# Performance work log

Measured on AMD Instinct MI355X. Metric: run time of the kernel, lower is better.

Reference implementation:

```python
import jax, jax.numpy as jnp
import numpy as np

IN_F = 1024
OUT_F = 1024
DEGREE = 7  # degree+1 = 8 Chebyshev terms


def setup_inputs() -> dict:
    key = jax.random.key(0)
    k1, k2, k3 = jax.random.split(key, 3)
    x = jax.random.normal(k1, (16384, IN_F), dtype=jnp.float32)
    std = 1.0 / (IN_F * (DEGREE + 1))
    cheby_coeffs = jax.random.normal(k2, (OUT_F, IN_F, DEGREE + 1), dtype=jnp.float32) * std
    # xavier_uniform for base_weight [out, in]
    limit = float(np.sqrt(6.0 / (IN_F + OUT_F)))
    base_weight = jax.random.uniform(k3, (OUT_F, IN_F), dtype=jnp.float32, minval=-limit, maxval=limit)
    return {"x": x, "cheby_coeffs": cheby_coeffs, "base_weight": base_weight}


def _cheby_basis(x_norm, degree):
    terms = [jnp.ones_like(x_norm), x_norm]
    for _ in range(2, degree + 1):
        terms.append(2.0 * x_norm * terms[-1] - terms[-2])
    return jnp.stack(terms, axis=-1)  # [b, i, d+1]


def reference(x, cheby_coeffs, base_weight):
    x_norm = jnp.tanh(x)
    basis = _cheby_basis(x_norm, DEGREE)               # [b, i, d]
    kan_out = jnp.einsum('bid,oid->bo', basis, cheby_coeffs)
    base_out = x @ base_weight.T                        # F.linear
    return kan_out + base_out
```

## Files before the change

kernel.cpp:

```cpp
#include <hip/hip_runtime.h>
#include <hip/hip_bf16.h>
#include <stdint.h>

typedef short short8 __attribute__((ext_vector_type(8)));
typedef float f32x16 __attribute__((ext_vector_type(16)));

#define KD 8192
#define NT 128

__device__ __forceinline__ unsigned short bfb(float f) {
    __hip_bfloat16 h = __float2bfloat16(f);
    return __builtin_bit_cast(unsigned short, h);
}

__device__ __forceinline__ short8 cheby8(float xv) {
    float e  = __builtin_amdgcn_exp2f(xv * 2.8853900817779268f);
    float xn = 1.0f - 2.0f * __builtin_amdgcn_rcpf(1.0f + e);
    float x2 = xn + xn;
    float t2 = x2 * xn - 1.0f;
    float t3 = x2 * t2 - xn;
    float t4 = x2 * t3 - t2;
    float t5 = x2 * t4 - t3;
    float t6 = x2 * t5 - t4;
    float t7 = x2 * t6 - t5;
    short8 v;
    v[0] = bfb(xv); v[1] = bfb(xn); v[2] = bfb(t2); v[3] = bfb(t3);
    v[4] = bfb(t4); v[5] = bfb(t5); v[6] = bfb(t6); v[7] = bfb(t7);
    return v;
}

__global__ void prep_w(const float* __restrict__ C, const float* __restrict__ W,
                       unsigned short* __restrict__ Bw) {
    int g = blockIdx.x * 256 + threadIdx.x;
    int o = g >> 10, i = g & 1023;
    const float* src = C + ((size_t)o * 8192 + i * 8);
    float4 v0 = *(const float4*)src;
    float4 v1 = *(const float4*)(src + 4);
    v0.x = W[o * 1024 + i];
    short8 r;
    r[0] = bfb(v0.x); r[1] = bfb(v0.y); r[2] = bfb(v0.z); r[3] = bfb(v0.w);
    r[4] = bfb(v1.x); r[5] = bfb(v1.y); r[6] = bfb(v1.z); r[7] = bfb(v1.w);
    *(short8*)(Bw + (size_t)g * 8) = r;
}

__global__ void prep_bias(const float* __restrict__ C, float* __restrict__ bias) {
    int o = blockIdx.x;
    int tid = threadIdx.x;
    float s = 0.f;
    for (int i = tid; i < 1024; i += 256)
        s += C[(size_t)o * 8192 + (size_t)i * 8];
    #pragma unroll
    for (int off = 32; off > 0; off >>= 1) s += __shfl_down(s, off);
    __shared__ float red[4];
    if ((tid & 63) == 0) red[tid >> 6] = s;
    __syncthreads();
    if (tid == 0) bias[o] = red[0] + red[1] + red[2] + red[3];
}


#define GLDS(NXT_, C_, TT_) \
    __builtin_amdgcn_global_load_lds( \
        (const __attribute__((address_space(1))) unsigned int*)((const char*)Bw + boff[C_] + (size_t)(TT_) * 128), \
        (__attribute__((address_space(3))) unsigned int*)(&Bs[NXT_][(wave * 4 + (C_)) * 8][0]), 16, 0, 0)

#define XLOAD(DST_, TI_) { \
    const float* ap_ = xbase + (size_t)(TI_) * 8; \
    asm volatile("global_load_dwordx4 %0, %1, off" : "=&v"(DST_) : "v"(ap_)); }

#define PHASE(CUR_, KK_) { \
    const int fb_ = (KK_) * 2 + lg; \
    const int co_ = (fb_ ^ (lr & 7)) * 16; \
    short8 a0_ = *(const short8*)((const char*)&As[CUR_][0][0] + (wm +  0 + lr) * 128 + co_); \
    short8 a1_ = *(const short8*)((const char*)&As[CUR_][0][0] + (wm + 32 + lr) * 128 + co_); \
    short8 a2_ = *(const short8*)((const char*)&As[CUR_][0][0] + (wm + 64 + lr) * 128 + co_); \
    short8 a3_ = *(const short8*)((const char*)&As[CUR_][0][0] + (wm + 96 + lr) * 128 + co_); \
    short8 b0_ = *(const short8*)((const char*)&Bs[CUR_][0][0] + (wn +  0 + lr) * 128 + co_); \
    short8 b1_ = *(const short8*)((const char*)&Bs[CUR_][0][0] + (wn + 32 + lr) * 128 + co_); \
    __builtin_amdgcn_s_setprio(1); \
    acc[0][0] = __builtin_amdgcn_mfma_f32_32x32x16_bf16(a0_, b0_, acc[0][0], 0, 0, 0); \
    acc[0][1] = __builtin_amdgcn_mfma_f32_32x32x16_bf16(a0_, b1_, acc[0][1], 0, 0, 0); \
    acc[1][0] = __builtin_amdgcn_mfma_f32_32x32x16_bf16(a1_, b0_, acc[1][0], 0, 0, 0); \
    acc[1][1] = __builtin_amdgcn_mfma_f32_32x32x16_bf16(a1_, b1_, acc[1][1], 0, 0, 0); \
    acc[2][0] = __builtin_amdgcn_mfma_f32_32x32x16_bf16(a2_, b0_, acc[2][0], 0, 0, 0); \
    acc[2][1] = __builtin_amdgcn_mfma_f32_32x32x16_bf16(a2_, b1_, acc[2][1], 0, 0, 0); \
    acc[3][0] = __builtin_amdgcn_mfma_f32_32x32x16_bf16(a3_, b0_, acc[3][0], 0, 0, 0); \
    acc[3][1] = __builtin_amdgcn_mfma_f32_32x32x16_bf16(a3_, b1_, acc[3][1], 0, 0, 0); \
    __builtin_amdgcn_s_setprio(0); \
}

#define CHEBY_STAGE(NXT_, XV_) { \
    short8 c0_ = cheby8(XV_.x); \
    short8 c1_ = cheby8(XV_.y); \
    short8 c2_ = cheby8(XV_.z); \
    short8 c3_ = cheby8(XV_.w); \
    *(short8*)((char*)&As[NXT_][0][0] + woff[0]) = c0_; \
    *(short8*)((char*)&As[NXT_][0][0] + woff[1]) = c1_; \
    *(short8*)((char*)&As[NXT_][0][0] + woff[2]) = c2_; \
    *(short8*)((char*)&As[NXT_][0][0] + woff[3]) = c3_; \
}

#define TILE(CUR_, NXT_, T_, XU_, XL_) { \
    const int tn_ = ((T_) + 1 < NT) ? (T_) + 1 : NT - 1; \
    const int tl_ = ((T_) + 2 < NT) ? (T_) + 2 : NT - 1; \
    GLDS(NXT_, 0, tn_); GLDS(NXT_, 1, tn_); GLDS(NXT_, 2, tn_); GLDS(NXT_, 3, tn_); \
    XLOAD(XL_, tl_) \
    PHASE(CUR_, 0) \
    PHASE(CUR_, 1) \
    asm volatile("s_waitcnt vmcnt(5)" ::: "memory");  \
    __builtin_amdgcn_sched_barrier(0); \
    CHEBY_STAGE(NXT_, XU_) \
    PHASE(CUR_, 2) \
    PHASE(CUR_, 3) \
    asm volatile("s_waitcnt vmcnt(1)" ::: "memory");  \
    __builtin_amdgcn_sched_barrier(0); \
    asm volatile("s_waitcnt lgkmcnt(0)" ::: "memory");  \
    __builtin_amdgcn_s_barrier(); \
    __builtin_amdgcn_sched_barrier(0); \
}

__global__ __launch_bounds__(512, 2)
void cheby_gemm(const float* __restrict__ X, const unsigned short* __restrict__ Bw,
                const float* __restrict__ bias, float* __restrict__ Out) {
    __shared__ unsigned short As[2][256][64];
    __shared__ unsigned short Bs[2][256][64];

    const int tid  = threadIdx.x;
    const int lane = tid & 63;
    const int wave = tid >> 6;

    int bid = blockIdx.x;
    int lin = (bid & 7) * 32 + (bid >> 3);
    const int m0 = (lin & 63) << 8;
    const int n0 = (lin >> 6) << 8;

    const int wm = (wave >> 2) * 128;
    const int wn = (wave & 3) * 64;
    const int lr = lane & 31;
    const int lg = lane >> 5;

    const int arow = tid >> 1;
    const int xf   = (tid & 1) * 4;
    const float* xbase = X + (size_t)(m0 + arow) * 1024 + xf;
    unsigned int woff[4];
    #pragma unroll
    for (int j = 0; j < 4; ++j)
        woff[j] = (unsigned)(arow * 128 + (((xf + j) ^ (arow & 7)) * 16));

    unsigned int boff[4];
    #pragma unroll
    for (int c = 0; c < 4; ++c) {
        int row   = (wave * 4 + c) * 8 + (lane >> 3);
        int chunk = (lane & 7) ^ (lane >> 3);
        boff[c] = ((unsigned)(n0 + row) * 8192u + (unsigned)chunk * 8u) * 2u;
    }

    f32x16 acc[4][2] = {};
    float4 xr0, xr1;

    {
        XLOAD(xr0, 0)
        GLDS(0, 0, 0); GLDS(0, 1, 0); GLDS(0, 2, 0); GLDS(0, 3, 0);
        XLOAD(xr1, 1)
        asm volatile("s_waitcnt vmcnt(5)" ::: "memory");
        __builtin_amdgcn_sched_barrier(0);
        CHEBY_STAGE(0, xr0)
        asm volatile("s_waitcnt vmcnt(1)" ::: "memory");
        __builtin_amdgcn_sched_barrier(0);
        asm volatile("s_waitcnt lgkmcnt(0)" ::: "memory");
        __builtin_amdgcn_s_barrier();
        __builtin_amdgcn_sched_barrier(0);
    }

    for (int t = 0; t < NT; t += 2) {
        TILE(0, 1, t,     xr1, xr0)
        TILE(1, 0, t + 1, xr0, xr1)
    }

    #pragma unroll
    for (int ni = 0; ni < 2; ++ni) {
        int col = n0 + wn + ni * 32 + lr;
        float bv = bias[col];
        #pragma unroll
        for (int mi = 0; mi < 4; ++mi) {
            #pragma unroll
            for (int r = 0; r < 16; ++r) {
                int row = m0 + wm + mi * 32 + 4 * lg + (r & 3) + 8 * (r >> 2);
                Out[(size_t)row * 1024 + col] = acc[mi][ni][r] + bv;
            }
        }
    }
}

extern "C" void kernel_launch(void* const* d_in, const int* in_sizes, int n_in,
                              void* d_out, int out_size, void* d_ws, size_t ws_size,
                              hipStream_t stream) {
    const float* x = (const float*)d_in[0];
    const float* C = (const float*)d_in[1];
    const float* W = (const float*)d_in[2];
    float* out = (float*)d_out;

    unsigned short* Bw = (unsigned short*)d_ws;
    float* bias = (float*)((char*)d_ws + (size_t)16 * 1024 * 1024);

    prep_w<<<4096, 256, 0, stream>>>(C, W, Bw);
    prep_bias<<<1024, 256, 0, stream>>>(C, bias);
    cheby_gemm<<<256, 512, 0, stream>>>(x, Bw, bias, out);
}
```

Before: 297.6 us.

## Pre-tile weights into k-chunk-major layout and drop LDS XOR swizzle

The weight prep kernel now writes the bf16 weight matrix in a tiled layout ordered by N-tile, K-tile and 8-element chunk, with 256 columns contiguous per chunk. Global-to-LDS copies become fully contiguous 32KB blocks per tile, and the A and B shared tiles are indexed as [chunk][row] short8 arrays instead of row-major with an XOR swizzle. This simplifies address arithmetic and makes the B loads coalesced, but the MFMA fragment reads and the Chebyshev stores now use a different LDS access pattern. That pattern could change bank-conflict behaviour.

```diff
diff --git a/kernel.cpp b/kernel.cpp
--- a/kernel.cpp
+++ b/kernel.cpp
@@ -40,7 +40,9 @@
     short8 r;
     r[0] = bfb(v0.x); r[1] = bfb(v0.y); r[2] = bfb(v0.z); r[3] = bfb(v0.w);
     r[4] = bfb(v1.x); r[5] = bfb(v1.y); r[6] = bfb(v1.z); r[7] = bfb(v1.w);
-    *(short8*)(Bw + (size_t)g * 8) = r;
+    int nt = o >> 8, col = o & 255, t = i >> 3, f = i & 7;
+    size_t dst16 = ((size_t)(nt * 128 + t) * 8 + f) * 256 + col;
+    *(short8*)(Bw + dst16 * 8) = r;
 }
 
 __global__ void prep_bias(const float* __restrict__ C, float* __restrict__ bias) {
@@ -60,22 +62,22 @@
 
 #define GLDS(NXT_, C_, TT_) \
     __builtin_amdgcn_global_load_lds( \
-        (const __attribute__((address_space(1))) unsigned int*)((const char*)Bw + boff[C_] + (size_t)(TT_) * 128), \
-        (__attribute__((address_space(3))) unsigned int*)(&Bs[NXT_][(wave * 4 + (C_)) * 8][0]), 16, 0, 0)
+        (const __attribute__((address_space(1))) unsigned int*)(Bw_byte + (size_t)(TT_) * 32768 + boff[C_]), \
+        (__attribute__((address_space(3))) unsigned int*)((unsigned short*)&Bs[NXT_][0] + (wave * 4 + (C_)) * 512), \
+        16, 0, 0)
 
 #define XLOAD(DST_, TI_) { \
     const float* ap_ = xbase + (size_t)(TI_) * 8; \
     asm volatile("global_load_dwordx4 %0, %1, off" : "=&v"(DST_) : "v"(ap_)); }
 
 #define PHASE(CUR_, KK_) { \
-    const int fb_ = (KK_) * 2 + lg; \
-    const int co_ = (fb_ ^ (lr & 7)) * 16; \
-    short8 a0_ = *(const short8*)((const char*)&As[CUR_][0][0] + (wm +  0 + lr) * 128 + co_); \
-    short8 a1_ = *(const short8*)((const char*)&As[CUR_][0][0] + (wm + 32 + lr) * 128 + co_); \
-    short8 a2_ = *(const short8*)((const char*)&As[CUR_][0][0] + (wm + 64 + lr) * 128 + co_); \
-    short8 a3_ = *(const short8*)((const char*)&As[CUR_][0][0] + (wm + 96 + lr) * 128 + co_); \
-    short8 b0_ = *(const short8*)((const char*)&Bs[CUR_][0][0] + (wn +  0 + lr) * 128 + co_); \
-    short8 b1_ = *(const short8*)((const char*)&Bs[CUR_][0][0] + (wn + 32 + lr) * 128 + co_); \
+    const int fo_ = ((KK_) * 2 + lg) * 256 + lr;   \
+    short8 a0_ = As[CUR_][fo_ + wm +  0]; \
+    short8 a1_ = As[CUR_][fo_ + wm + 32]; \
+    short8 a2_ = As[CUR_][fo_ + wm + 64]; \
+    short8 a3_ = As[CUR_][fo_ + wm + 96]; \
+    short8 b0_ = Bs[CUR_][fo_ + wn +  0]; \
+    short8 b1_ = Bs[CUR_][fo_ + wn + 32]; \
     __builtin_amdgcn_s_setprio(1); \
     acc[0][0] = __builtin_amdgcn_mfma_f32_32x32x16_bf16(a0_, b0_, acc[0][0], 0, 0, 0); \
     acc[0][1] = __builtin_amdgcn_mfma_f32_32x32x16_bf16(a0_, b1_, acc[0][1], 0, 0, 0); \
@@ -89,14 +91,10 @@
 }
 
 #define CHEBY_STAGE(NXT_, XV_) { \
-    short8 c0_ = cheby8(XV_.x); \
-    short8 c1_ = cheby8(XV_.y); \
-    short8 c2_ = cheby8(XV_.z); \
-    short8 c3_ = cheby8(XV_.w); \
-    *(short8*)((char*)&As[NXT_][0][0] + woff[0]) = c0_; \
-    *(short8*)((char*)&As[NXT_][0][0] + woff[1]) = c1_; \
-    *(short8*)((char*)&As[NXT_][0][0] + woff[2]) = c2_; \
-    *(short8*)((char*)&As[NXT_][0][0] + woff[3]) = c3_; \
+    As[NXT_][woff0 +   0] = cheby8(XV_.x); \
+    As[NXT_][woff0 + 256] = cheby8(XV_.y); \
+    As[NXT_][woff0 + 512] = cheby8(XV_.z); \
+    As[NXT_][woff0 + 768] = cheby8(XV_.w); \
 }
 
 #define TILE(CUR_, NXT_, T_, XU_, XL_) { \
@@ -121,8 +119,8 @@
 __global__ __launch_bounds__(512, 2)
 void cheby_gemm(const float* __restrict__ X, const unsigned short* __restrict__ Bw,
                 const float* __restrict__ bias, float* __restrict__ Out) {
-    __shared__ unsigned short As[2][256][64];
-    __shared__ unsigned short Bs[2][256][64];
+    __shared__ short8 As[2][2048];
+    __shared__ short8 Bs[2][2048];
 
     const int tid  = threadIdx.x;
     const int lane = tid & 63;
@@ -141,18 +139,13 @@
     const int arow = tid >> 1;
     const int xf   = (tid & 1) * 4;
     const float* xbase = X + (size_t)(m0 + arow) * 1024 + xf;
-    unsigned int woff[4];
-    #pragma unroll
-    for (int j = 0; j < 4; ++j)
-        woff[j] = (unsigned)(arow * 128 + (((xf + j) ^ (arow & 7)) * 16));
-
+    const int woff0 = xf * 256 + arow;
+
+    const char* Bw_byte = (const char*)Bw + (size_t)(n0 >> 8) * 4194304;
     unsigned int boff[4];
     #pragma unroll
-    for (int c = 0; c < 4; ++c) {
-        int row   = (wave * 4 + c) * 8 + (lane >> 3);
-        int chunk = (lane & 7) ^ (lane >> 3);
-        boff[c] = ((unsigned)(n0 + row) * 8192u + (unsigned)chunk * 8u) * 2u;
-    }
+    for (int c = 0; c < 4; ++c)
+        boff[c] = (unsigned)(((wave * 4 + c) * 64 + lane) * 16);
 
     f32x16 acc[4][2] = {};
     float4 xr0, xr1;
```

Measured after the change: 287.0 us. 1.04x faster.
